# Optimization experiments

Measured on AMD Instinct MI355X. Metric: run time of the kernel, lower is better.

## Reference

```python
import jax, jax.numpy as jnp
import numpy as np

N_NODES = 100000
DIM = 64
N_EDGES = 1250000
PRESERVE = 0.1  # preserve_ratio in GCN module


def gcn_conv(x, W, b, row, col, edge_w, num_nodes):
    """PyG GCNConv with normalize=True: symmetric norm with added self-loops.
    x: [N, d], W: [d, d_out], edge (row -> col) with weight edge_w: [E].
    """
    # add self-loops with weight 1
    loop = jnp.arange(num_nodes, dtype=row.dtype)
    r = jnp.concatenate([row, loop])
    c = jnp.concatenate([col, loop])
    w = jnp.concatenate([edge_w, jnp.ones((num_nodes,), dtype=edge_w.dtype)])
    # symmetric degree normalization: deg computed at target (col)
    deg = jax.ops.segment_sum(w, c, num_segments=num_nodes)
    dinv = jnp.where(deg > 0, jax.lax.rsqrt(deg), 0.0)
    norm = dinv[r] * w * dinv[c]  # [E+N]
    xw = x @ W  # [N, d_out] (linear transform before propagation)
    msg = xw[r] * norm[:, None]  # gather + scale
    out = jax.ops.segment_sum(msg, c, num_segments=num_nodes)  # scatter-add at targets
    return out + b


def setup_inputs() -> dict:
    key = jax.random.key(0)
    ks = jax.random.split(key, 8)
    skill_embed = jax.random.normal(ks[0], (N_NODES, DIM), dtype=jnp.float32)
    edge_index = jax.random.randint(ks[1], (2, N_EDGES), 0, N_NODES, dtype=jnp.int64)
    edge_attr = jax.random.uniform(ks[2], (N_EDGES,), dtype=jnp.float32)
    # GCNConv params (W stored as [in, out] here), glorot-ish init
    scale = 1.0 / np.sqrt(DIM)
    W1 = jax.random.uniform(ks[3], (DIM, DIM), minval=-scale, maxval=scale, dtype=jnp.float32)
    b1 = jnp.zeros((DIM,), dtype=jnp.float32)
    W2 = jax.random.uniform(ks[4], (DIM, DIM), minval=-scale, maxval=scale, dtype=jnp.float32)
    b2 = jnp.zeros((DIM,), dtype=jnp.float32)
    return {"skill_embed": skill_embed, "edge_index": edge_index, "edge_attr": edge_attr,
            "W1": W1, "b1": b1, "W2": W2, "b2": b2}


def reference(skill_embed, edge_index, edge_attr, W1, b1, W2, b2):
    row, col = edge_index[0], edge_index[1]
    n = skill_embed.shape[0]
    temp = skill_embed
    out = gcn_conv(skill_embed, W1, b1, row, col, edge_attr, n)
    temp = (1.0 - PRESERVE) * out + PRESERVE * temp
    out = gcn_conv(temp, W2, b2, row, col, edge_attr, n)
    temp = (1.0 - PRESERVE) * out + PRESERVE * temp
    return temp
```

## Files before the change

kernel.cpp:

```cpp
#include <hip/hip_runtime.h>

#define DIM 64
#define PRESERVE 0.1f
#define P_BLK 1024
#define BSH 7
#define BNODES 128
#define NBMAX 1024
#define ROWB 20
#define ROWM ((1 << ROWB) - 1)

static_assert(BNODES == (1 << BSH), "bucket geometry");
static_assert((1 << ROWB) >= 131072, "row must fit in ROWB bits for N<=131072");

typedef unsigned short bf16_t;

__device__ __forceinline__ float readlane_f(float v, int l) {
    return __int_as_float(__builtin_amdgcn_readlane(__float_as_int(v), l));
}
__device__ __forceinline__ float bf2f(bf16_t u) {
    return __uint_as_float(((unsigned)u) << 16);
}
__device__ __forceinline__ bf16_t f2bf(float f) {
    unsigned u = __float_as_uint(f);
    unsigned r = (u + 0x7FFFu + ((u >> 16) & 1u)) >> 16;
    return (bf16_t)r;
}


__global__ __launch_bounds__(256) void k_bcount(const int* __restrict__ col,
                                                int* __restrict__ bh,
                                                int E, int nb, int chunk) {
    __shared__ int hist[NBMAX];
    int t = threadIdx.x;
    for (int i = t; i < nb; i += 256) hist[i] = 0;
    __syncthreads();
    int beg = blockIdx.x * chunk;
    int end = beg + chunk;
    if (end > E) end = E;
    for (int i = beg + t; i < end; i += 256) atomicAdd(&hist[col[i] >> BSH], 1);
    __syncthreads();
    size_t base = (size_t)blockIdx.x * nb;
    for (int i = t; i < nb; i += 256) bh[base + i] = hist[i];
}

__global__ __launch_bounds__(256) void k_bscan1(const int* __restrict__ bh,
                                                int* __restrict__ bh2,
                                                int* __restrict__ btot, int nb) {
    __shared__ int s[256];
    int t = threadIdx.x;
    int i = blockIdx.x;
    int v0 = bh[(size_t)(t * 4 + 0) * nb + i];
    int v1 = bh[(size_t)(t * 4 + 1) * nb + i];
    int v2 = bh[(size_t)(t * 4 + 2) * nb + i];
    int v3 = bh[(size_t)(t * 4 + 3) * nb + i];
    int sum = v0 + v1 + v2 + v3;
    s[t] = sum;
    __syncthreads();
    for (int off = 1; off < 256; off <<= 1) {
        int x = (t >= off) ? s[t - off] : 0;
        __syncthreads();
        s[t] += x;
        __syncthreads();
    }
    int run = s[t] - sum;
    size_t ob = (size_t)i * P_BLK + t * 4;
    bh2[ob + 0] = run; run += v0;
    bh2[ob + 1] = run; run += v1;
    bh2[ob + 2] = run; run += v2;
    bh2[ob + 3] = run;
    if (t == 255) btot[i] = s[255];
}

__global__ __launch_bounds__(1024) void k_bscan2(const int* __restrict__ btot,
                                                 int* __restrict__ bbase,
                                                 int nb, int E) {
    __shared__ int s[1024];
    int t = threadIdx.x;
    int v = (t < nb) ? btot[t] : 0;
    s[t] = v;
    __syncthreads();
    for (int off = 1; off < 1024; off <<= 1) {
        int x = (t >= off) ? s[t - off] : 0;
        __syncthreads();
        s[t] += x;
        __syncthreads();
    }
    if (t < nb) bbase[t] = s[t] - v;
    if (t == 0) bbase[nb] = E;
}

__global__ __launch_bounds__(256) void k_bscatter(
        const int* __restrict__ row, const int* __restrict__ col,
        const float* __restrict__ ew, const int* __restrict__ bh2,
        const int* __restrict__ bbase, int2* __restrict__ sered,
        int E, int nb, int chunk) {
    __shared__ int cur[NBMAX];
    int t = threadIdx.x;
    int blk = blockIdx.x;
    for (int i = t; i < nb; i += 256)
        cur[i] = bbase[i] + bh2[(size_t)i * P_BLK + blk];
    __syncthreads();
    int beg = blk * chunk;
    int end = beg + chunk;
    if (end > E) end = E;
    for (int i = beg + t; i < end; i += 256) {
        int c = col[i];
        int r = row[i];
        float w = ew[i];
        int slot = atomicAdd(&cur[c >> BSH], 1);
        int2 p;
        p.x = r | ((c & (BNODES - 1)) << ROWB);
        p.y = __float_as_int(w);
        sered[slot] = p;
    }
}

__global__ __launch_bounds__(256) void k_bcsr(
        const int2* __restrict__ sered, const int* __restrict__ bbase,
        int2* __restrict__ sedge, int* __restrict__ offsets,
        float* __restrict__ dinv, int N, int E) {
    __shared__ int cnt[BNODES];
    __shared__ float degw[BNODES];
    __shared__ int sc[BNODES];
    __shared__ int cur[BNODES];
    int t = threadIdx.x;
    int b = blockIdx.x;
    if (t < BNODES) { cnt[t] = 0; degw[t] = 0.0f; }
    __syncthreads();
    int s0 = bbase[b];
    int e0 = bbase[b + 1];
    for (int i = s0 + t; i < e0; i += 256) {
        int2 p = sered[i];
        int loc = ((unsigned)p.x) >> ROWB;
        atomicAdd(&cnt[loc], 1);
        atomicAdd(&degw[loc], __int_as_float(p.y));
    }
    __syncthreads();
    if (t < BNODES) sc[t] = cnt[t];
    __syncthreads();
    for (int off = 1; off < BNODES; off <<= 1) {
        int x = 0;
        if (t < BNODES && t >= off) x = sc[t - off];
        __syncthreads();
        if (t < BNODES) sc[t] += x;
        __syncthreads();
    }
    if (t < BNODES) {
        int excl = sc[t] - cnt[t];
        cur[t] = excl;
        int node = (b << BSH) + t;
        if (node < N) {
            offsets[node] = s0 + excl;
            dinv[node] = rsqrtf(1.0f + degw[t]);
        }
    }
    if (b == 0 && t == 0) offsets[N] = E;
    __syncthreads();
    for (int i = s0 + t; i < e0; i += 256) {
        int2 p = sered[i];
        int loc = ((unsigned)p.x) >> ROWB;
        int slot = atomicAdd(&cur[loc], 1);
        int2 q;
        q.x = p.x & ROWM;
        q.y = p.y;
        sedge[s0 + slot] = q;
    }
}

__global__ __launch_bounds__(256) void k_mm(
        const float* __restrict__ x, const float* __restrict__ W,
        const float* __restrict__ dinv, bf16_t* __restrict__ xs, int n) {
    int tid = threadIdx.x;
    int lane = tid & 63;
    int waveId = blockIdx.x * 4 + (tid >> 6);
    int nWaves = gridDim.x * 4;

    float Wr[DIM];
#pragma unroll
    for (int k = 0; k < DIM; ++k) Wr[k] = W[k * DIM + lane];

    for (int r0 = waveId * 4; r0 < n; r0 += nWaves * 4) {
        if (r0 + 3 < n) {
            float x0 = x[(size_t)(r0 + 0) * DIM + lane];
            float x1 = x[(size_t)(r0 + 1) * DIM + lane];
            float x2 = x[(size_t)(r0 + 2) * DIM + lane];
            float x3 = x[(size_t)(r0 + 3) * DIM + lane];
            float a0 = 0.f, a1 = 0.f, a2 = 0.f, a3 = 0.f;
#pragma unroll
            for (int k = 0; k < DIM; ++k) {
                float w = Wr[k];
                a0 += readlane_f(x0, k) * w;
                a1 += readlane_f(x1, k) * w;
                a2 += readlane_f(x2, k) * w;
                a3 += readlane_f(x3, k) * w;
            }
            xs[(size_t)(r0 + 0) * DIM + lane] = f2bf(a0 * dinv[r0 + 0]);
            xs[(size_t)(r0 + 1) * DIM + lane] = f2bf(a1 * dinv[r0 + 1]);
            xs[(size_t)(r0 + 2) * DIM + lane] = f2bf(a2 * dinv[r0 + 2]);
            xs[(size_t)(r0 + 3) * DIM + lane] = f2bf(a3 * dinv[r0 + 3]);
        } else {
            for (int r = r0; r < n; ++r) {
                float xv = x[(size_t)r * DIM + lane];
                float a = 0.f;
#pragma unroll
                for (int k = 0; k < DIM; ++k) a += readlane_f(xv, k) * Wr[k];
                xs[(size_t)r * DIM + lane] = f2bf(a * dinv[r]);
            }
        }
    }
}

__global__ __launch_bounds__(256) void k_gather(
        const bf16_t* __restrict__ xs, const int* __restrict__ offsets,
        const int2* __restrict__ sedge, const float* __restrict__ dinv,
        const float* __restrict__ b, const float* __restrict__ xprev,
        float* __restrict__ out, int n) {
    int tid = threadIdx.x;
    int lane = tid & 63;
    int c = blockIdx.x * 4 + (tid >> 6);
    if (c >= n) return;
    float di = dinv[c];
    float xp = xprev[(size_t)c * DIM + lane];
    float bl = b[lane];
    float acc0 = bf2f(xs[(size_t)c * DIM + lane]);
    float acc1 = 0.0f;
    int beg = offsets[c];
    int end = offsets[c + 1];
    for (int b0 = beg; b0 < end; b0 += 64) {
        int m = end - b0;
        if (m > 64) m = 64;
        int r_l = 0, w_l = 0;
        if (lane < m) {
            int2 p = sedge[b0 + lane];
            r_l = p.x;
            w_l = p.y;
        }
        int j = 0;
        for (; j + 7 < m; j += 8) {
            int k0 = __builtin_amdgcn_readlane(r_l, j);
            int k1 = __builtin_amdgcn_readlane(r_l, j + 1);
            int k2 = __builtin_amdgcn_readlane(r_l, j + 2);
            int k3 = __builtin_amdgcn_readlane(r_l, j + 3);
            int k4 = __builtin_amdgcn_readlane(r_l, j + 4);
            int k5 = __builtin_amdgcn_readlane(r_l, j + 5);
            int k6 = __builtin_amdgcn_readlane(r_l, j + 6);
            int k7 = __builtin_amdgcn_readlane(r_l, j + 7);
            float w0 = readlane_f(__int_as_float(w_l), j);
            float w1 = readlane_f(__int_as_float(w_l), j + 1);
            float w2 = readlane_f(__int_as_float(w_l), j + 2);
            float w3 = readlane_f(__int_as_float(w_l), j + 3);
            float w4 = readlane_f(__int_as_float(w_l), j + 4);
            float w5 = readlane_f(__int_as_float(w_l), j + 5);
            float w6 = readlane_f(__int_as_float(w_l), j + 6);
            float w7 = readlane_f(__int_as_float(w_l), j + 7);
            float a0 = bf2f(xs[(size_t)k0 * DIM + lane]);
            float a1 = bf2f(xs[(size_t)k1 * DIM + lane]);
            float a2 = bf2f(xs[(size_t)k2 * DIM + lane]);
            float a3 = bf2f(xs[(size_t)k3 * DIM + lane]);
            float a4 = bf2f(xs[(size_t)k4 * DIM + lane]);
            float a5 = bf2f(xs[(size_t)k5 * DIM + lane]);
            float a6 = bf2f(xs[(size_t)k6 * DIM + lane]);
            float a7 = bf2f(xs[(size_t)k7 * DIM + lane]);
            acc0 += a0 * w0;
            acc1 += a1 * w1;
            acc0 += a2 * w2;
            acc1 += a3 * w3;
            acc0 += a4 * w4;
            acc1 += a5 * w5;
            acc0 += a6 * w6;
            acc1 += a7 * w7;
        }
        for (; j + 3 < m; j += 4) {
            int k0 = __builtin_amdgcn_readlane(r_l, j);
            int k1 = __builtin_amdgcn_readlane(r_l, j + 1);
            int k2 = __builtin_amdgcn_readlane(r_l, j + 2);
            int k3 = __builtin_amdgcn_readlane(r_l, j + 3);
            float w0 = readlane_f(__int_as_float(w_l), j);
            float w1 = readlane_f(__int_as_float(w_l), j + 1);
            float w2 = readlane_f(__int_as_float(w_l), j + 2);
            float w3 = readlane_f(__int_as_float(w_l), j + 3);
            float a0 = bf2f(xs[(size_t)k0 * DIM + lane]);
            float a1 = bf2f(xs[(size_t)k1 * DIM + lane]);
            float a2 = bf2f(xs[(size_t)k2 * DIM + lane]);
            float a3 = bf2f(xs[(size_t)k3 * DIM + lane]);
            acc0 += a0 * w0;
            acc1 += a1 * w1;
            acc0 += a2 * w2;
            acc1 += a3 * w3;
        }
        for (; j < m; ++j) {
            int k0 = __builtin_amdgcn_readlane(r_l, j);
            float w0 = readlane_f(__int_as_float(w_l), j);
            acc0 += bf2f(xs[(size_t)k0 * DIM + lane]) * w0;
        }
    }
    float acc = acc0 + acc1;
    float v = (1.0f - PRESERVE) * (acc * di + bl) + PRESERVE * xp;
    out[(size_t)c * DIM + lane] = v;
}

extern "C" void kernel_launch(void* const* d_in, const int* in_sizes, int n_in,
                              void* d_out, int out_size, void* d_ws, size_t ws_size,
                              hipStream_t stream) {
    const float* x  = (const float*)d_in[0];
    const int*   ei = (const int*)d_in[1];
    const float* ew = (const float*)d_in[2];
    const float* W1 = (const float*)d_in[3];
    const float* b1 = (const float*)d_in[4];
    const float* W2 = (const float*)d_in[5];
    const float* b2 = (const float*)d_in[6];

    const int N = in_sizes[0] / DIM;
    const int E = in_sizes[2];
    const int* row = ei;
    const int* col = ei + E;

    const int nb = (N + BNODES - 1) >> BSH;
    const int chunk = (E + P_BLK - 1) / P_BLK;

    int2* sedge   = (int2*)d_ws;
    float* dinv   = (float*)(sedge + E);
    bf16_t* xs    = (bf16_t*)(dinv + N);
    int* offsets  = (int*)(xs + (size_t)N * DIM);
    int* btot     = offsets + N + 1;
    int* bbase    = btot + nb;
    size_t toff = (size_t)((char*)(bbase + nb + 1) - (char*)d_ws);
    toff = (toff + 255) & ~(size_t)255;
    float* temp   = (float*)((char*)d_ws + toff);
    int* bh2      = (int*)temp;
    int* bh       = bh2 + (size_t)nb * P_BLK;
    int2* sered   = (int2*)(bh + (size_t)P_BLK * nb);

    const int B = 256;
    const int nblkG = (N + 3) / 4;
    const int nblkMM = 1024;

    k_bcount<<<P_BLK, B, 0, stream>>>(col, bh, E, nb, chunk);
    k_bscan1<<<nb, B, 0, stream>>>(bh, bh2, btot, nb);
    k_bscan2<<<1, 1024, 0, stream>>>(btot, bbase, nb, E);
    k_bscatter<<<P_BLK, B, 0, stream>>>(row, col, ew, bh2, bbase, sered, E, nb, chunk);
    k_bcsr<<<nb, B, 0, stream>>>(sered, bbase, sedge, offsets, dinv, N, E);

    k_mm<<<nblkMM, B, 0, stream>>>(x, W1, dinv, xs, N);
    k_gather<<<nblkG, B, 0, stream>>>(xs, offsets, sedge, dinv, b1, x, temp, N);

    k_mm<<<nblkMM, B, 0, stream>>>(temp, W2, dinv, xs, N);
    k_gather<<<nblkG, B, 0, stream>>>(xs, offsets, sedge, dinv, b2, temp, (float*)d_out, N);
}
```

Before: 275.5 us.

## Process two nodes per wavefront in gather and double bucket-sort partitions

The gather kernel now has each wavefront handle two destination nodes and interleave their edge streams, so more independent feature loads are in flight per wave. The bucket histogram uses twice as many partition blocks, which means smaller chunks, and the prefix-scan output layout is transposed so that the scatter kernel reads its offsets contiguously. The aim is to hide gather latency and speed up the sort preprocessing, at the cost of more registers, divergence between the two nodes' unequal degrees, and a larger histogram scan.

Measured after the change: 285.4 us. +3.6%, slower.

```diff
diff --git a/kernel.cpp b/kernel.cpp
--- a/kernel.cpp
+++ b/kernel.cpp
@@ -2,7 +2,7 @@
 
 #define DIM 64
 #define PRESERVE 0.1f
-#define P_BLK 1024
+#define P_BLK 2048
 #define BSH 7
 #define BNODES 128
 #define NBMAX 1024
@@ -49,11 +49,13 @@
     __shared__ int s[256];
     int t = threadIdx.x;
     int i = blockIdx.x;
-    int v0 = bh[(size_t)(t * 4 + 0) * nb + i];
-    int v1 = bh[(size_t)(t * 4 + 1) * nb + i];
-    int v2 = bh[(size_t)(t * 4 + 2) * nb + i];
-    int v3 = bh[(size_t)(t * 4 + 3) * nb + i];
-    int sum = v0 + v1 + v2 + v3;
+    int v[8];
+    int sum = 0;
+#pragma unroll
+    for (int q = 0; q < 8; ++q) {
+        v[q] = bh[(size_t)(t * 8 + q) * nb + i];
+        sum += v[q];
+    }
     s[t] = sum;
     __syncthreads();
     for (int off = 1; off < 256; off <<= 1) {
@@ -63,11 +65,11 @@
         __syncthreads();
     }
     int run = s[t] - sum;
-    size_t ob = (size_t)i * P_BLK + t * 4;
-    bh2[ob + 0] = run; run += v0;
-    bh2[ob + 1] = run; run += v1;
-    bh2[ob + 2] = run; run += v2;
-    bh2[ob + 3] = run;
+#pragma unroll
+    for (int q = 0; q < 8; ++q) {
+        bh2[(size_t)(t * 8 + q) * nb + i] = run;
+        run += v[q];
+    }
     if (t == 255) btot[i] = s[255];
 }
 
@@ -97,8 +99,9 @@
     __shared__ int cur[NBMAX];
     int t = threadIdx.x;
     int blk = blockIdx.x;
+    size_t hb = (size_t)blk * nb;
     for (int i = t; i < nb; i += 256)
-        cur[i] = bbase[i] + bh2[(size_t)i * P_BLK + blk];
+        cur[i] = bbase[i] + bh2[hb + i];
     __syncthreads();
     int beg = blk * chunk;
     int end = beg + chunk;
@@ -217,86 +220,128 @@
         float* __restrict__ out, int n) {
     int tid = threadIdx.x;
     int lane = tid & 63;
-    int c = blockIdx.x * 4 + (tid >> 6);
-    if (c >= n) return;
-    float di = dinv[c];
-    float xp = xprev[(size_t)c * DIM + lane];
+    int wv = blockIdx.x * 4 + (tid >> 6);
+    int c0 = wv * 2;
+    if (c0 >= n) return;
+    int c1 = c0 + 1;
     float bl = b[lane];
-    float acc0 = bf2f(xs[(size_t)c * DIM + lane]);
-    float acc1 = 0.0f;
-    int beg = offsets[c];
-    int end = offsets[c + 1];
-    for (int b0 = beg; b0 < end; b0 += 64) {
-        int m = end - b0;
-        if (m > 64) m = 64;
-        int r_l = 0, w_l = 0;
-        if (lane < m) {
-            int2 p = sedge[b0 + lane];
-            r_l = p.x;
-            w_l = p.y;
-        }
-        int j = 0;
-        for (; j + 7 < m; j += 8) {
-            int k0 = __builtin_amdgcn_readlane(r_l, j);
-            int k1 = __builtin_amdgcn_readlane(r_l, j + 1);
-            int k2 = __builtin_amdgcn_readlane(r_l, j + 2);
-            int k3 = __builtin_amdgcn_readlane(r_l, j + 3);
-            int k4 = __builtin_amdgcn_readlane(r_l, j + 4);
-            int k5 = __builtin_amdgcn_readlane(r_l, j + 5);
-            int k6 = __builtin_amdgcn_readlane(r_l, j + 6);
-            int k7 = __builtin_amdgcn_readlane(r_l, j + 7);
-            float w0 = readlane_f(__int_as_float(w_l), j);
-            float w1 = readlane_f(__int_as_float(w_l), j + 1);
-            float w2 = readlane_f(__int_as_float(w_l), j + 2);
-            float w3 = readlane_f(__int_as_float(w_l), j + 3);
-            float w4 = readlane_f(__int_as_float(w_l), j + 4);
-            float w5 = readlane_f(__int_as_float(w_l), j + 5);
-            float w6 = readlane_f(__int_as_float(w_l), j + 6);
-            float w7 = readlane_f(__int_as_float(w_l), j + 7);
-            float a0 = bf2f(xs[(size_t)k0 * DIM + lane]);
-            float a1 = bf2f(xs[(size_t)k1 * DIM + lane]);
-            float a2 = bf2f(xs[(size_t)k2 * DIM + lane]);
-            float a3 = bf2f(xs[(size_t)k3 * DIM + lane]);
-            float a4 = bf2f(xs[(size_t)k4 * DIM + lane]);
-            float a5 = bf2f(xs[(size_t)k5 * DIM + lane]);
-            float a6 = bf2f(xs[(size_t)k6 * DIM + lane]);
-            float a7 = bf2f(xs[(size_t)k7 * DIM + lane]);
-            acc0 += a0 * w0;
-            acc1 += a1 * w1;
-            acc0 += a2 * w2;
-            acc1 += a3 * w3;
-            acc0 += a4 * w4;
-            acc1 += a5 * w5;
-            acc0 += a6 * w6;
-            acc1 += a7 * w7;
-        }
-        for (; j + 3 < m; j += 4) {
-            int k0 = __builtin_amdgcn_readlane(r_l, j);
-            int k1 = __builtin_amdgcn_readlane(r_l, j + 1);
-            int k2 = __builtin_amdgcn_readlane(r_l, j + 2);
-            int k3 = __builtin_amdgcn_readlane(r_l, j + 3);
-            float w0 = readlane_f(__int_as_float(w_l), j);
-            float w1 = readlane_f(__int_as_float(w_l), j + 1);
-            float w2 = readlane_f(__int_as_float(w_l), j + 2);
-            float w3 = readlane_f(__int_as_float(w_l), j + 3);
-            float a0 = bf2f(xs[(size_t)k0 * DIM + lane]);
-            float a1 = bf2f(xs[(size_t)k1 * DIM + lane]);
-            float a2 = bf2f(xs[(size_t)k2 * DIM + lane]);
-            float a3 = bf2f(xs[(size_t)k3 * DIM + lane]);
-            acc0 += a0 * w0;
-            acc1 += a1 * w1;
-            acc0 += a2 * w2;
-            acc1 += a3 * w3;
-        }
-        for (; j < m; ++j) {
-            int k0 = __builtin_amdgcn_readlane(r_l, j);
-            float w0 = readlane_f(__int_as_float(w_l), j);
-            acc0 += bf2f(xs[(size_t)k0 * DIM + lane]) * w0;
-        }
-    }
-    float acc = acc0 + acc1;
-    float v = (1.0f - PRESERVE) * (acc * di + bl) + PRESERVE * xp;
-    out[(size_t)c * DIM + lane] = v;
+    float di0 = dinv[c0];
+    float xp0 = xprev[(size_t)c0 * DIM + lane];
+    float acc0 = bf2f(xs[(size_t)c0 * DIM + lane]);
+    float acc0b = 0.f, acc1b = 0.f;
+    int beg0 = offsets[c0];
+    int end0 = offsets[c0 + 1];
+    float di1 = 0.f, xp1 = 0.f, acc1 = 0.f;
+    int beg1 = end0, end1 = end0;
+    if (c1 < n) {
+        di1 = dinv[c1];
+        xp1 = xprev[(size_t)c1 * DIM + lane];
+        acc1 = bf2f(xs[(size_t)c1 * DIM + lane]);
+        end1 = offsets[c1 + 1];
+    }
+    int b0 = beg0, b1 = beg1;
+    while (b0 < end0 || b1 < end1) {
+        int m0 = end0 - b0; m0 = m0 < 0 ? 0 : (m0 > 64 ? 64 : m0);
+        int m1 = end1 - b1; m1 = m1 < 0 ? 0 : (m1 > 64 ? 64 : m1);
+        int r0l = 0, w0l = 0, r1l = 0, w1l = 0;
+        if (lane < m0) { int2 p = sedge[b0 + lane]; r0l = p.x; w0l = p.y; }
+        if (lane < m1) { int2 p = sedge[b1 + lane]; r1l = p.x; w1l = p.y; }
+        int j0 = 0, j1 = 0;
+        while (j0 + 3 < m0 && j1 + 3 < m1) {
+            int k00 = __builtin_amdgcn_readlane(r0l, j0);
+            int k01 = __builtin_amdgcn_readlane(r0l, j0 + 1);
+            int k02 = __builtin_amdgcn_readlane(r0l, j0 + 2);
+            int k03 = __builtin_amdgcn_readlane(r0l, j0 + 3);
+            int k10 = __builtin_amdgcn_readlane(r1l, j1);
+            int k11 = __builtin_amdgcn_readlane(r1l, j1 + 1);
+            int k12 = __builtin_amdgcn_readlane(r1l, j1 + 2);
+            int k13 = __builtin_amdgcn_readlane(r1l, j1 + 3);
+            float w00 = readlane_f(__int_as_float(w0l), j0);
+            float w01 = readlane_f(__int_as_float(w0l), j0 + 1);
+            float w02 = readlane_f(__int_as_float(w0l), j0 + 2);
+            float w03 = readlane_f(__int_as_float(w0l), j0 + 3);
+            float w10 = readlane_f(__int_as_float(w1l), j1);
+            float w11 = readlane_f(__int_as_float(w1l), j1 + 1);
+            float w12 = readlane_f(__int_as_float(w1l), j1 + 2);
+            float w13 = readlane_f(__int_as_float(w1l), j1 + 3);
+            float a00 = bf2f(xs[(size_t)k00 * DIM + lane]);
+            float a01 = bf2f(xs[(size_t)k01 * DIM + lane]);
+            float a02 = bf2f(xs[(size_t)k02 * DIM + lane]);
+            float a03 = bf2f(xs[(size_t)k03 * DIM + lane]);
+            float a10 = bf2f(xs[(size_t)k10 * DIM + lane]);
+            float a11 = bf2f(xs[(size_t)k11 * DIM + lane]);
+            float a12 = bf2f(xs[(size_t)k12 * DIM + lane]);
+            float a13 = bf2f(xs[(size_t)k13 * DIM + lane]);
+            acc0 += a00 * w00;
+            acc0b += a01 * w01;
+            acc0 += a02 * w02;
+            acc0b += a03 * w03;
+            acc1 += a10 * w10;
+            acc1b += a11 * w11;
+            acc1 += a12 * w12;
+            acc1b += a13 * w13;
+            j0 += 4;
+            j1 += 4;
+        }
+        while (j0 + 3 < m0) {
+            int k00 = __builtin_amdgcn_readlane(r0l, j0);
+            int k01 = __builtin_amdgcn_readlane(r0l, j0 + 1);
+            int k02 = __builtin_amdgcn_readlane(r0l, j0 + 2);
+            int k03 = __builtin_amdgcn_readlane(r0l, j0 + 3);
+            float w00 = readlane_f(__int_as_float(w0l), j0);
+            float w01 = readlane_f(__int_as_float(w0l), j0 + 1);
+            float w02 = readlane_f(__int_as_float(w0l), j0 + 2);
+            float w03 = readlane_f(__int_as_float(w0l), j0 + 3);
+            float a00 = bf2f(xs[(size_t)k00 * DIM + lane]);
+            float a01 = bf2f(xs[(size_t)k01 * DIM + lane]);
+            float a02 = bf2f(xs[(size_t)k02 * DIM + lane]);
+            float a03 = bf2f(xs[(size_t)k03 * DIM + lane]);
+            acc0 += a00 * w00;
+            acc0b += a01 * w01;
+            acc0 += a02 * w02;
+            acc0b += a03 * w03;
+            j0 += 4;
+        }
+        while (j1 + 3 < m1) {
+            int k10 = __builtin_amdgcn_readlane(r1l, j1);
+            int k11 = __builtin_amdgcn_readlane(r1l, j1 + 1);
+            int k12 = __builtin_amdgcn_readlane(r1l, j1 + 2);
+            int k13 = __builtin_amdgcn_readlane(r1l, j1 + 3);
+            float w10 = readlane_f(__int_as_float(w1l), j1);
+            float w11 = readlane_f(__int_as_float(w1l), j1 + 1);
+            float w12 = readlane_f(__int_as_float(w1l), j1 + 2);
+            float w13 = readlane_f(__int_as_float(w1l), j1 + 3);
+            float a10 = bf2f(xs[(size_t)k10 * DIM + lane]);
+            float a11 = bf2f(xs[(size_t)k11 * DIM + lane]);
+            float a12 = bf2f(xs[(size_t)k12 * DIM + lane]);
+            float a13 = bf2f(xs[(size_t)k13 * DIM + lane]);
+            acc1 += a10 * w10;
+            acc1b += a11 * w11;
+            acc1 += a12 * w12;
+            acc1b += a13 * w13;
+            j1 += 4;
+        }
+        for (; j0 < m0; ++j0) {
+            int k00 = __builtin_amdgcn_readlane(r0l, j0);
+            float w00 = readlane_f(__int_as_float(w0l), j0);
+            acc0 += bf2f(xs[(size_t)k00 * DIM + lane]) * w00;
+        }
+        for (; j1 < m1; ++j1) {
+            int k10 = __builtin_amdgcn_readlane(r1l, j1);
+            float w10 = readlane_f(__int_as_float(w1l), j1);
+            acc1 += bf2f(xs[(size_t)k10 * DIM + lane]) * w10;
+        }
+        b0 += m0;
+        b1 += m1;
+    }
+    float s0 = acc0 + acc0b;
+    out[(size_t)c0 * DIM + lane] =
+        (1.0f - PRESERVE) * (s0 * di0 + bl) + PRESERVE * xp0;
+    if (c1 < n) {
+        float s1 = acc1 + acc1b;
+        out[(size_t)c1 * DIM + lane] =
+            (1.0f - PRESERVE) * (s1 * di1 + bl) + PRESERVE * xp1;
+    }
 }
 
 extern "C" void kernel_launch(void* const* d_in, const int* in_sizes, int n_in,
@@ -328,11 +373,11 @@
     toff = (toff + 255) & ~(size_t)255;
     float* temp   = (float*)((char*)d_ws + toff);
     int* bh2      = (int*)temp;
-    int* bh       = bh2 + (size_t)nb * P_BLK;
+    int* bh       = bh2 + (size_t)P_BLK * nb;
     int2* sered   = (int2*)(bh + (size_t)P_BLK * nb);
 
     const int B = 256;
-    const int nblkG = (N + 3) / 4;
+    const int nblkG = (N + 7) / 8;
     const int nblkMM = 1024;
 
     k_bcount<<<P_BLK, B, 0, stream>>>(col, bh, E, nb, chunk);
```
